# Kernel optimization log

Hardware: AMD Instinct MI355X
Metric: run time of the kernel (lower is better)

Reference implementation:

```python
import jax, jax.numpy as jnp
import numpy as np
from jax import lax

INPUT, HIDDEN, OUT = 64, 128, 40
B, T = 256, 512


def _lstm_layer(x, Wih, Whh, bih, bhh):
    # x: [B, T, D]; PyTorch gate order: i, f, g, o in stacked [4H, .] weights
    Bsz = x.shape[0]
    H = Whh.shape[1]
    b = bih + bhh

    def step(carry, xt):
        h, c = carry
        gates = xt @ Wih.T + h @ Whh.T + b  # [B, 4H]
        i, f, g, o = jnp.split(gates, 4, axis=-1)
        i = jax.nn.sigmoid(i)
        f = jax.nn.sigmoid(f)
        g = jnp.tanh(g)
        o = jax.nn.sigmoid(o)
        c = f * c + i * g
        h = o * jnp.tanh(c)
        return (h, c), h

    init = (jnp.zeros((Bsz, H), x.dtype), jnp.zeros((Bsz, H), x.dtype))
    (h_last, _), ys = lax.scan(step, init, jnp.swapaxes(x, 0, 1))
    return jnp.swapaxes(ys, 0, 1), h_last


def setup_inputs() -> dict:
    key = jax.random.key(0)
    ks = jax.random.split(key, 11)
    s_in = 1.0 / np.sqrt(HIDDEN)
    u = lambda k, shp: jax.random.uniform(k, shp, jnp.float32, -s_in, s_in)
    return {
        "x": jax.random.normal(ks[0], (B, T, INPUT), jnp.float32),
        "Wih0": u(ks[1], (4 * HIDDEN, INPUT)),
        "Whh0": u(ks[2], (4 * HIDDEN, HIDDEN)),
        "bih0": u(ks[3], (4 * HIDDEN,)),
        "bhh0": u(ks[4], (4 * HIDDEN,)),
        "Wih1": u(ks[5], (4 * HIDDEN, HIDDEN)),
        "Whh1": u(ks[6], (4 * HIDDEN, HIDDEN)),
        "bih1": u(ks[7], (4 * HIDDEN,)),
        "bhh1": u(ks[8], (4 * HIDDEN,)),
        "Wfc": u(ks[9], (OUT, HIDDEN)),
        "bfc": u(ks[10], (OUT,)),
    }


def reference(x, Wih0, Whh0, bih0, bhh0, Wih1, Whh1, bih1, bhh1, Wfc, bfc):
    y0, _ = _lstm_layer(x, Wih0, Whh0, bih0, bhh0)        # [B, T, H]
    _, h_last = _lstm_layer(y0, Wih1, Whh1, bih1, bhh1)   # [B, H] == y[:, -1]
    return h_last @ Wfc.T + bfc                            # [B, 40]
```

## Files before the change

kernel.cpp:

```cpp
#include <hip/hip_runtime.h>

#define BATCH 256
#define TLEN  512
#define DIN   64
#define HID   128
#define NOUT  40
#define SC    16

typedef _Float16 f16x8 __attribute__((ext_vector_type(8)));
typedef float    f32x4 __attribute__((ext_vector_type(4)));

#define MFMA16(a, b, c) __builtin_amdgcn_mfma_f32_16x16x32_f16((a), (b), (c), 0, 0, 0)

#define BARRIER() do {                                      \
    asm volatile("s_waitcnt lgkmcnt(0)" ::: "memory");      \
    __builtin_amdgcn_s_barrier();                           \
} while (0)

static __device__ __forceinline__ f16x8 pack8(float4 a, float4 b) {
    f16x8 v;
    v[0] = (_Float16)a.x; v[1] = (_Float16)a.y; v[2] = (_Float16)a.z; v[3] = (_Float16)a.w;
    v[4] = (_Float16)b.x; v[5] = (_Float16)b.y; v[6] = (_Float16)b.z; v[7] = (_Float16)b.w;
    return v;
}
static __device__ __forceinline__ float sig_(float x) {
    return __builtin_amdgcn_rcpf(1.0f + __expf(-x));
}
static __device__ __forceinline__ float tanh_(float x) {
    return fmaf(-2.0f, __builtin_amdgcn_rcpf(__expf(2.0f * x) + 1.0f), 1.0f);
}
static __device__ __forceinline__ f32x4 splat4(float v) { return (f32x4){v, v, v, v}; }

#define LD8(base, g, K, kt) pack8(*(const float4*)((base) + (size_t)(g) * (K) + (kt) * 32 + kg * 8), \
                                  *(const float4*)((base) + (size_t)(g) * (K) + (kt) * 32 + kg * 8 + 4))

#define H_STEP_CORE(SL, P)                                                      \
    f32x4 xi = *(const f32x4*)&xacc[((SL) * HID + hid) * 4];                    \
    const _Float16* hb = &h_lds[P][0];                                          \
    f16x8 h0 = *(const f16x8*)(hb + kg * 8);                                    \
    f16x8 h1 = *(const f16x8*)(hb + 32 + kg * 8);                               \
    f16x8 h2 = *(const f16x8*)(hb + 64 + kg * 8);                               \
    f16x8 h3 = *(const f16x8*)(hb + 96 + kg * 8);                               \
    f32x4 a0 = MFMA16(h0, Wh00, xi);                                            \
    f32x4 a1 = MFMA16(h0, Wh10, splat4(xi[1]));                                 \
    f32x4 a2 = MFMA16(h0, Wh20, splat4(xi[2]));                                 \
    f32x4 a3 = MFMA16(h0, Wh30, splat4(xi[3]));                                 \
    a0 = MFMA16(h1, Wh01, a0); a1 = MFMA16(h1, Wh11, a1);                       \
    a2 = MFMA16(h1, Wh21, a2); a3 = MFMA16(h1, Wh31, a3);                       \
    a0 = MFMA16(h2, Wh02, a0); a1 = MFMA16(h2, Wh12, a1);                       \
    a2 = MFMA16(h2, Wh22, a2); a3 = MFMA16(h2, Wh32, a3);                       \
    a0 = MFMA16(h3, Wh03, a0); a1 = MFMA16(h3, Wh13, a1);                       \
    a2 = MFMA16(h3, Wh23, a2); a3 = MFMA16(h3, Wh33, a3);                       \
    float iv = sig_(a0[0]), fv = sig_(a1[0]);                                   \
    float gv = tanh_(a2[0]), ov = sig_(a3[0]);                                  \
    cc = fmaf(fv, cc, iv * gv);                                                 \
    hv = ov * tanh_(cc);

__global__ void __attribute__((amdgpu_flat_work_group_size(512, 512), amdgpu_waves_per_eu(2, 2)))
lstm_l0(const float* __restrict__ x,
        const float* __restrict__ Wih, const float* __restrict__ Whh,
        const float* __restrict__ bih, const float* __restrict__ bhh,
        float* __restrict__ hstate, float* __restrict__ cstate,
        _Float16* __restrict__ y0, int t0, int t1)
{
    const int b    = blockIdx.x;
    const int tid  = threadIdx.x;
    const int lane = tid & 63;
    const int wave = tid >> 6;
    const int col  = lane & 15, kg = lane >> 4;
    const int hid  = wave * 16 + col;

    __shared__ __align__(16) float    xacc[SC * HID * 4];
    __shared__ __align__(16) _Float16 h_lds[2][HID];

    f16x8 Wx00 = LD8(Wih, 0 * HID + hid, DIN, 0), Wx01 = LD8(Wih, 0 * HID + hid, DIN, 1);
    f16x8 Wx10 = LD8(Wih, 1 * HID + hid, DIN, 0), Wx11 = LD8(Wih, 1 * HID + hid, DIN, 1);
    f16x8 Wx20 = LD8(Wih, 2 * HID + hid, DIN, 0), Wx21 = LD8(Wih, 2 * HID + hid, DIN, 1);
    f16x8 Wx30 = LD8(Wih, 3 * HID + hid, DIN, 0), Wx31 = LD8(Wih, 3 * HID + hid, DIN, 1);
    f16x8 Wh00 = LD8(Whh, 0 * HID + hid, HID, 0), Wh01 = LD8(Whh, 0 * HID + hid, HID, 1);
    f16x8 Wh02 = LD8(Whh, 0 * HID + hid, HID, 2), Wh03 = LD8(Whh, 0 * HID + hid, HID, 3);
    f16x8 Wh10 = LD8(Whh, 1 * HID + hid, HID, 0), Wh11 = LD8(Whh, 1 * HID + hid, HID, 1);
    f16x8 Wh12 = LD8(Whh, 1 * HID + hid, HID, 2), Wh13 = LD8(Whh, 1 * HID + hid, HID, 3);
    f16x8 Wh20 = LD8(Whh, 2 * HID + hid, HID, 0), Wh21 = LD8(Whh, 2 * HID + hid, HID, 1);
    f16x8 Wh22 = LD8(Whh, 2 * HID + hid, HID, 2), Wh23 = LD8(Whh, 2 * HID + hid, HID, 3);
    f16x8 Wh30 = LD8(Whh, 3 * HID + hid, HID, 0), Wh31 = LD8(Whh, 3 * HID + hid, HID, 1);
    f16x8 Wh32 = LD8(Whh, 3 * HID + hid, HID, 2), Wh33 = LD8(Whh, 3 * HID + hid, HID, 3);
    asm("" : "+a"(Wx00), "+a"(Wx01), "+a"(Wx10), "+a"(Wx11),
             "+a"(Wx20), "+a"(Wx21), "+a"(Wx30), "+a"(Wx31));
    asm("" : "+a"(Wh00), "+a"(Wh01), "+a"(Wh02), "+a"(Wh03),
             "+a"(Wh10), "+a"(Wh11), "+a"(Wh12), "+a"(Wh13));
    asm("" : "+a"(Wh20), "+a"(Wh21), "+a"(Wh22), "+a"(Wh23),
             "+a"(Wh30), "+a"(Wh31), "+a"(Wh32), "+a"(Wh33));

    const float bs0 = bih[0 * HID + hid] + bhh[0 * HID + hid];
    const float bs1 = bih[1 * HID + hid] + bhh[1 * HID + hid];
    const float bs2 = bih[2 * HID + hid] + bhh[2 * HID + hid];
    const float bs3 = bih[3 * HID + hid] + bhh[3 * HID + hid];

    float cc = cstate[(size_t)b * HID + hid];
    float hv = hstate[(size_t)b * HID + hid];
    if (kg == 0) h_lds[0][hid] = (_Float16)hv;

    const float* xA = x + (size_t)b * TLEN * DIN + (size_t)col * DIN + kg * 8;
    _Float16* y0p = y0 + (size_t)b * HID + hid;

    const int nt = t1 - t0;
    for (int sc = 0; sc < nt; sc += SC) {
        {
            const float* pa = xA + (size_t)(t0 + sc) * DIN;
            f16x8 A0 = pack8(*(const float4*)pa,        *(const float4*)(pa + 4));
            f16x8 A1 = pack8(*(const float4*)(pa + 32), *(const float4*)(pa + 36));
            f32x4 g0 = splat4(bs0), g1 = splat4(bs1), g2 = splat4(bs2), g3 = splat4(bs3);
            g0 = MFMA16(A0, Wx00, g0); g1 = MFMA16(A0, Wx10, g1);
            g2 = MFMA16(A0, Wx20, g2); g3 = MFMA16(A0, Wx30, g3);
            g0 = MFMA16(A1, Wx01, g0); g1 = MFMA16(A1, Wx11, g1);
            g2 = MFMA16(A1, Wx21, g2); g3 = MFMA16(A1, Wx31, g3);
            #pragma unroll
            for (int r = 0; r < 4; ++r) {
                const int tl = kg * 4 + r;
                float* d = &xacc[(tl * HID + hid) * 4];
                d[0] = g0[r]; d[1] = g1[r]; d[2] = g2[r]; d[3] = g3[r];
            }
        }
        BARRIER();
        for (int s = 0; s < SC; s += 2) {
            {
                H_STEP_CORE(s, 0)
                if (kg == 0) {
                    h_lds[1][hid] = (_Float16)hv;
                    y0p[(size_t)(sc + s) * (BATCH * HID)] = (_Float16)hv;
                }
                BARRIER();
            }
            {
                H_STEP_CORE(s + 1, 1)
                if (kg == 0) {
                    h_lds[0][hid] = (_Float16)hv;
                    y0p[(size_t)(sc + s + 1) * (BATCH * HID)] = (_Float16)hv;
                }
                BARRIER();
            }
        }
    }
    if (kg == 0) {
        cstate[(size_t)b * HID + hid] = cc;
        hstate[(size_t)b * HID + hid] = hv;
    }
}

__global__ void __attribute__((amdgpu_flat_work_group_size(512, 512), amdgpu_waves_per_eu(2, 2)))
lstm_l1(const _Float16* __restrict__ y0in,
        const float* __restrict__ Wih, const float* __restrict__ Whh,
        const float* __restrict__ bih, const float* __restrict__ bhh,
        float* __restrict__ hstate, float* __restrict__ cstate,
        int t0, int t1)
{
    const int b    = blockIdx.x;
    const int tid  = threadIdx.x;
    const int lane = tid & 63;
    const int wave = tid >> 6;
    const int col  = lane & 15, kg = lane >> 4;
    const int hid  = wave * 16 + col;

    __shared__ __align__(16) float    xacc[SC * HID * 4];
    __shared__ __align__(16) _Float16 h_lds[2][HID];

    f16x8 Wh00 = LD8(Whh, 0 * HID + hid, HID, 0), Wh01 = LD8(Whh, 0 * HID + hid, HID, 1);
    f16x8 Wh02 = LD8(Whh, 0 * HID + hid, HID, 2), Wh03 = LD8(Whh, 0 * HID + hid, HID, 3);
    f16x8 Wh10 = LD8(Whh, 1 * HID + hid, HID, 0), Wh11 = LD8(Whh, 1 * HID + hid, HID, 1);
    f16x8 Wh12 = LD8(Whh, 1 * HID + hid, HID, 2), Wh13 = LD8(Whh, 1 * HID + hid, HID, 3);
    f16x8 Wh20 = LD8(Whh, 2 * HID + hid, HID, 0), Wh21 = LD8(Whh, 2 * HID + hid, HID, 1);
    f16x8 Wh22 = LD8(Whh, 2 * HID + hid, HID, 2), Wh23 = LD8(Whh, 2 * HID + hid, HID, 3);
    f16x8 Wh30 = LD8(Whh, 3 * HID + hid, HID, 0), Wh31 = LD8(Whh, 3 * HID + hid, HID, 1);
    f16x8 Wh32 = LD8(Whh, 3 * HID + hid, HID, 2), Wh33 = LD8(Whh, 3 * HID + hid, HID, 3);
    asm("" : "+a"(Wh00), "+a"(Wh01), "+a"(Wh02), "+a"(Wh03),
             "+a"(Wh10), "+a"(Wh11), "+a"(Wh12), "+a"(Wh13));
    asm("" : "+a"(Wh20), "+a"(Wh21), "+a"(Wh22), "+a"(Wh23),
             "+a"(Wh30), "+a"(Wh31), "+a"(Wh32), "+a"(Wh33));

    const float bs0 = bih[0 * HID + hid] + bhh[0 * HID + hid];
    const float bs1 = bih[1 * HID + hid] + bhh[1 * HID + hid];
    const float bs2 = bih[2 * HID + hid] + bhh[2 * HID + hid];
    const float bs3 = bih[3 * HID + hid] + bhh[3 * HID + hid];

    float cc = cstate[(size_t)b * HID + hid];
    float hv = hstate[(size_t)b * HID + hid];
    if (kg == 0) h_lds[0][hid] = (_Float16)hv;

    const _Float16* yA = y0in + ((size_t)col * BATCH + b) * HID + kg * 8;

    const int nt = t1 - t0;
    for (int sc = 0; sc < nt; sc += SC) {
        {
            f16x8 Wy00 = LD8(Wih, 0 * HID + hid, HID, 0), Wy01 = LD8(Wih, 0 * HID + hid, HID, 1);
            f16x8 Wy02 = LD8(Wih, 0 * HID + hid, HID, 2), Wy03 = LD8(Wih, 0 * HID + hid, HID, 3);
            f16x8 Wy10 = LD8(Wih, 1 * HID + hid, HID, 0), Wy11 = LD8(Wih, 1 * HID + hid, HID, 1);
            f16x8 Wy12 = LD8(Wih, 1 * HID + hid, HID, 2), Wy13 = LD8(Wih, 1 * HID + hid, HID, 3);
            f16x8 Wy20 = LD8(Wih, 2 * HID + hid, HID, 0), Wy21 = LD8(Wih, 2 * HID + hid, HID, 1);
            f16x8 Wy22 = LD8(Wih, 2 * HID + hid, HID, 2), Wy23 = LD8(Wih, 2 * HID + hid, HID, 3);
            f16x8 Wy30 = LD8(Wih, 3 * HID + hid, HID, 0), Wy31 = LD8(Wih, 3 * HID + hid, HID, 1);
            f16x8 Wy32 = LD8(Wih, 3 * HID + hid, HID, 2), Wy33 = LD8(Wih, 3 * HID + hid, HID, 3);
            const _Float16* pa = yA + (size_t)sc * (BATCH * HID);
            f16x8 A0 = *(const f16x8*)(pa);
            f16x8 A1 = *(const f16x8*)(pa + 32);
            f16x8 A2 = *(const f16x8*)(pa + 64);
            f16x8 A3 = *(const f16x8*)(pa + 96);
            f32x4 g0 = splat4(bs0), g1 = splat4(bs1), g2 = splat4(bs2), g3 = splat4(bs3);
            g0 = MFMA16(A0, Wy00, g0); g1 = MFMA16(A0, Wy10, g1);
            g2 = MFMA16(A0, Wy20, g2); g3 = MFMA16(A0, Wy30, g3);
            g0 = MFMA16(A1, Wy01, g0); g1 = MFMA16(A1, Wy11, g1);
            g2 = MFMA16(A1, Wy21, g2); g3 = MFMA16(A1, Wy31, g3);
            g0 = MFMA16(A2, Wy02, g0); g1 = MFMA16(A2, Wy12, g1);
            g2 = MFMA16(A2, Wy22, g2); g3 = MFMA16(A2, Wy32, g3);
            g0 = MFMA16(A3, Wy03, g0); g1 = MFMA16(A3, Wy13, g1);
            g2 = MFMA16(A3, Wy23, g2); g3 = MFMA16(A3, Wy33, g3);
            #pragma unroll
            for (int r = 0; r < 4; ++r) {
                const int tl = kg * 4 + r;
                float* d = &xacc[(tl * HID + hid) * 4];
                d[0] = g0[r]; d[1] = g1[r]; d[2] = g2[r]; d[3] = g3[r];
            }
        }
        BARRIER();
        for (int s = 0; s < SC; s += 2) {
            {
                H_STEP_CORE(s, 0)
                if (kg == 0) h_lds[1][hid] = (_Float16)hv;
                BARRIER();
            }
            {
                H_STEP_CORE(s + 1, 1)
                if (kg == 0) h_lds[0][hid] = (_Float16)hv;
                BARRIER();
            }
        }
    }
    if (kg == 0) {
        cstate[(size_t)b * HID + hid] = cc;
        hstate[(size_t)b * HID + hid] = hv;
    }
}

__global__ __launch_bounds__(128) void fc_kernel(
    const float* __restrict__ h1, const float* __restrict__ Wfc,
    const float* __restrict__ bfc, float* __restrict__ out)
{
    const int b = blockIdx.x;
    const int o = threadIdx.x;
    __shared__ float hs[HID];
    hs[o] = h1[(size_t)b * HID + o];
    __syncthreads();
    if (o < NOUT) {
        const float4* w  = reinterpret_cast<const float4*>(Wfc + (size_t)o * HID);
        const float4* hv = reinterpret_cast<const float4*>(hs);
        float acc = bfc[o];
        #pragma unroll
        for (int q = 0; q < HID / 4; ++q) {
            float4 wv = w[q]; float4 h4 = hv[q];
            acc = fmaf(wv.x, h4.x, fmaf(wv.y, h4.y, fmaf(wv.z, h4.z, fmaf(wv.w, h4.w, acc))));
        }
        out[(size_t)b * NOUT + o] = acc;
    }
}

extern "C" void kernel_launch(void* const* d_in, const int* in_sizes, int n_in,
                              void* d_out, int out_size, void* d_ws, size_t ws_size,
                              hipStream_t stream) {
    const float* x    = (const float*)d_in[0];
    const float* Wih0 = (const float*)d_in[1];
    const float* Whh0 = (const float*)d_in[2];
    const float* bih0 = (const float*)d_in[3];
    const float* bhh0 = (const float*)d_in[4];
    const float* Wih1 = (const float*)d_in[5];
    const float* Whh1 = (const float*)d_in[6];
    const float* bih1 = (const float*)d_in[7];
    const float* bhh1 = (const float*)d_in[8];
    const float* Wfc  = (const float*)d_in[9];
    const float* bfc  = (const float*)d_in[10];
    float* out = (float*)d_out;

    float* hst0 = (float*)d_ws;
    float* cst0 = hst0 + BATCH * HID;
    float* hst1 = cst0 + BATCH * HID;
    float* cst1 = hst1 + BATCH * HID;
    _Float16* y0 = (_Float16*)(cst1 + BATCH * HID);

    const size_t stateBytes = (size_t)4 * BATCH * HID * sizeof(float);
    size_t avail = ws_size > stateBytes ? ws_size - stateBytes : 0;
    int Tc = (int)(avail / ((size_t)BATCH * HID * 2));
    if (Tc > TLEN) Tc = TLEN;
    Tc &= ~(SC - 1);
    if (Tc < SC) Tc = SC;

    hipMemsetAsync(d_ws, 0, stateBytes, stream);

    for (int t0 = 0; t0 < TLEN; t0 += Tc) {
        int t1 = t0 + Tc; if (t1 > TLEN) t1 = TLEN;
        lstm_l0<<<BATCH, 512, 0, stream>>>(x, Wih0, Whh0, bih0, bhh0, hst0, cst0, y0, t0, t1);
        lstm_l1<<<BATCH, 512, 0, stream>>>(y0, Wih1, Whh1, bih1, bhh1, hst1, cst1, t0, t1);
    }
    fc_kernel<<<BATCH, 128, 0, stream>>>(hst1, Wfc, bfc, out);
}
```

Baseline: 578.3 us.

## Give each wave two hidden-unit tiles and halve the LSTM block size

Both LSTM kernels now launch 256 threads (4 waves) instead of 512. Each wave computes two 16-wide hidden tiles, and all weights for both tiles stay in AGPRs. The recurrent MFMAs now start from zero accumulators, with the input projection added at the gate activations, and the next step's input-projection values are prefetched from LDS during the current step. This is meant to cut barrier and synchronisation cost per timestep and to give each wave eight independent MFMA chains instead of four. The cost is twice as many MFMAs per wave on the serial critical path and higher register pressure.

```diff
diff --git a/kernel.cpp b/kernel.cpp
--- a/kernel.cpp
+++ b/kernel.cpp
@@ -34,29 +34,37 @@
 #define LD8(base, g, K, kt) pack8(*(const float4*)((base) + (size_t)(g) * (K) + (kt) * 32 + kg * 8), \
                                   *(const float4*)((base) + (size_t)(g) * (K) + (kt) * 32 + kg * 8 + 4))
 
-#define H_STEP_CORE(SL, P)                                                      \
-    f32x4 xi = *(const f32x4*)&xacc[((SL) * HID + hid) * 4];                    \
+#define HROUND(H, KT)                                                           \
+    aA0 = MFMA16(H, WhA0_##KT, aA0); aA1 = MFMA16(H, WhA1_##KT, aA1);           \
+    aA2 = MFMA16(H, WhA2_##KT, aA2); aA3 = MFMA16(H, WhA3_##KT, aA3);           \
+    aB0 = MFMA16(H, WhB0_##KT, aB0); aB1 = MFMA16(H, WhB1_##KT, aB1);           \
+    aB2 = MFMA16(H, WhB2_##KT, aB2); aB3 = MFMA16(H, WhB3_##KT, aB3);
+
+#define H_STEP_CORE(S, P, XIA, XIB, XIAN, XIBN)                                 \
     const _Float16* hb = &h_lds[P][0];                                          \
     f16x8 h0 = *(const f16x8*)(hb + kg * 8);                                    \
     f16x8 h1 = *(const f16x8*)(hb + 32 + kg * 8);                               \
     f16x8 h2 = *(const f16x8*)(hb + 64 + kg * 8);                               \
     f16x8 h3 = *(const f16x8*)(hb + 96 + kg * 8);                               \
-    f32x4 a0 = MFMA16(h0, Wh00, xi);                                            \
-    f32x4 a1 = MFMA16(h0, Wh10, splat4(xi[1]));                                 \
-    f32x4 a2 = MFMA16(h0, Wh20, splat4(xi[2]));                                 \
-    f32x4 a3 = MFMA16(h0, Wh30, splat4(xi[3]));                                 \
-    a0 = MFMA16(h1, Wh01, a0); a1 = MFMA16(h1, Wh11, a1);                       \
-    a2 = MFMA16(h1, Wh21, a2); a3 = MFMA16(h1, Wh31, a3);                       \
-    a0 = MFMA16(h2, Wh02, a0); a1 = MFMA16(h2, Wh12, a1);                       \
-    a2 = MFMA16(h2, Wh22, a2); a3 = MFMA16(h2, Wh32, a3);                       \
-    a0 = MFMA16(h3, Wh03, a0); a1 = MFMA16(h3, Wh13, a1);                       \
-    a2 = MFMA16(h3, Wh23, a2); a3 = MFMA16(h3, Wh33, a3);                       \
-    float iv = sig_(a0[0]), fv = sig_(a1[0]);                                   \
-    float gv = tanh_(a2[0]), ov = sig_(a3[0]);                                  \
-    cc = fmaf(fv, cc, iv * gv);                                                 \
-    hv = ov * tanh_(cc);
-
-__global__ void __attribute__((amdgpu_flat_work_group_size(512, 512), amdgpu_waves_per_eu(2, 2)))
+    { int sn = (S) + 1 < SC ? (S) + 1 : SC - 1;                                 \
+      XIAN = *(const f32x4*)&xacc[(sn * HID + hidA) * 4];                       \
+      XIBN = *(const f32x4*)&xacc[(sn * HID + hidB) * 4]; }                     \
+    f32x4 aA0 = z4, aA1 = z4, aA2 = z4, aA3 = z4;                               \
+    f32x4 aB0 = z4, aB1 = z4, aB2 = z4, aB3 = z4;                               \
+    HROUND(h0, 0)                                                               \
+    HROUND(h1, 1)                                                               \
+    HROUND(h2, 2)                                                               \
+    HROUND(h3, 3)                                                               \
+    float ivA = sig_(aA0[0] + XIA[0]), fvA = sig_(aA1[0] + XIA[1]);             \
+    float gvA = tanh_(aA2[0] + XIA[2]), ovA = sig_(aA3[0] + XIA[3]);            \
+    ccA = fmaf(fvA, ccA, ivA * gvA);                                            \
+    hvA = ovA * tanh_(ccA);                                                     \
+    float ivB = sig_(aB0[0] + XIB[0]), fvB = sig_(aB1[0] + XIB[1]);             \
+    float gvB = tanh_(aB2[0] + XIB[2]), ovB = sig_(aB3[0] + XIB[3]);            \
+    ccB = fmaf(fvB, ccB, ivB * gvB);                                            \
+    hvB = ovB * tanh_(ccB);
+
+__global__ void __attribute__((amdgpu_flat_work_group_size(256, 256), amdgpu_waves_per_eu(1, 1)))
 lstm_l0(const float* __restrict__ x,
         const float* __restrict__ Wih, const float* __restrict__ Whh,
         const float* __restrict__ bih, const float* __restrict__ bhh,
@@ -68,41 +76,70 @@
     const int lane = tid & 63;
     const int wave = tid >> 6;
     const int col  = lane & 15, kg = lane >> 4;
-    const int hid  = wave * 16 + col;
+    const int hidA = wave * 32 + col;
+    const int hidB = hidA + 16;
 
     __shared__ __align__(16) float    xacc[SC * HID * 4];
     __shared__ __align__(16) _Float16 h_lds[2][HID];
 
-    f16x8 Wx00 = LD8(Wih, 0 * HID + hid, DIN, 0), Wx01 = LD8(Wih, 0 * HID + hid, DIN, 1);
-    f16x8 Wx10 = LD8(Wih, 1 * HID + hid, DIN, 0), Wx11 = LD8(Wih, 1 * HID + hid, DIN, 1);
-    f16x8 Wx20 = LD8(Wih, 2 * HID + hid, DIN, 0), Wx21 = LD8(Wih, 2 * HID + hid, DIN, 1);
-    f16x8 Wx30 = LD8(Wih, 3 * HID + hid, DIN, 0), Wx31 = LD8(Wih, 3 * HID + hid, DIN, 1);
-    f16x8 Wh00 = LD8(Whh, 0 * HID + hid, HID, 0), Wh01 = LD8(Whh, 0 * HID + hid, HID, 1);
-    f16x8 Wh02 = LD8(Whh, 0 * HID + hid, HID, 2), Wh03 = LD8(Whh, 0 * HID + hid, HID, 3);
-    f16x8 Wh10 = LD8(Whh, 1 * HID + hid, HID, 0), Wh11 = LD8(Whh, 1 * HID + hid, HID, 1);
-    f16x8 Wh12 = LD8(Whh, 1 * HID + hid, HID, 2), Wh13 = LD8(Whh, 1 * HID + hid, HID, 3);
-    f16x8 Wh20 = LD8(Whh, 2 * HID + hid, HID, 0), Wh21 = LD8(Whh, 2 * HID + hid, HID, 1);
-    f16x8 Wh22 = LD8(Whh, 2 * HID + hid, HID, 2), Wh23 = LD8(Whh, 2 * HID + hid, HID, 3);
-    f16x8 Wh30 = LD8(Whh, 3 * HID + hid, HID, 0), Wh31 = LD8(Whh, 3 * HID + hid, HID, 1);
-    f16x8 Wh32 = LD8(Whh, 3 * HID + hid, HID, 2), Wh33 = LD8(Whh, 3 * HID + hid, HID, 3);
-    asm("" : "+a"(Wx00), "+a"(Wx01), "+a"(Wx10), "+a"(Wx11),
-             "+a"(Wx20), "+a"(Wx21), "+a"(Wx30), "+a"(Wx31));
-    asm("" : "+a"(Wh00), "+a"(Wh01), "+a"(Wh02), "+a"(Wh03),
-             "+a"(Wh10), "+a"(Wh11), "+a"(Wh12), "+a"(Wh13));
-    asm("" : "+a"(Wh20), "+a"(Wh21), "+a"(Wh22), "+a"(Wh23),
-             "+a"(Wh30), "+a"(Wh31), "+a"(Wh32), "+a"(Wh33));
-
-    const float bs0 = bih[0 * HID + hid] + bhh[0 * HID + hid];
-    const float bs1 = bih[1 * HID + hid] + bhh[1 * HID + hid];
-    const float bs2 = bih[2 * HID + hid] + bhh[2 * HID + hid];
-    const float bs3 = bih[3 * HID + hid] + bhh[3 * HID + hid];
-
-    float cc = cstate[(size_t)b * HID + hid];
-    float hv = hstate[(size_t)b * HID + hid];
-    if (kg == 0) h_lds[0][hid] = (_Float16)hv;
+    f16x8 WxA0_0 = LD8(Wih, 0 * HID + hidA, DIN, 0), WxA0_1 = LD8(Wih, 0 * HID + hidA, DIN, 1);
+    f16x8 WxA1_0 = LD8(Wih, 1 * HID + hidA, DIN, 0), WxA1_1 = LD8(Wih, 1 * HID + hidA, DIN, 1);
+    f16x8 WxA2_0 = LD8(Wih, 2 * HID + hidA, DIN, 0), WxA2_1 = LD8(Wih, 2 * HID + hidA, DIN, 1);
+    f16x8 WxA3_0 = LD8(Wih, 3 * HID + hidA, DIN, 0), WxA3_1 = LD8(Wih, 3 * HID + hidA, DIN, 1);
+    f16x8 WxB0_0 = LD8(Wih, 0 * HID + hidB, DIN, 0), WxB0_1 = LD8(Wih, 0 * HID + hidB, DIN, 1);
+    f16x8 WxB1_0 = LD8(Wih, 1 * HID + hidB, DIN, 0), WxB1_1 = LD8(Wih, 1 * HID + hidB, DIN, 1);
+    f16x8 WxB2_0 = LD8(Wih, 2 * HID + hidB, DIN, 0), WxB2_1 = LD8(Wih, 2 * HID + hidB, DIN, 1);
+    f16x8 WxB3_0 = LD8(Wih, 3 * HID + hidB, DIN, 0), WxB3_1 = LD8(Wih, 3 * HID + hidB, DIN, 1);
+    f16x8 WhA0_0 = LD8(Whh, 0 * HID + hidA, HID, 0), WhA0_1 = LD8(Whh, 0 * HID + hidA, HID, 1);
+    f16x8 WhA0_2 = LD8(Whh, 0 * HID + hidA, HID, 2), WhA0_3 = LD8(Whh, 0 * HID + hidA, HID, 3);
+    f16x8 WhA1_0 = LD8(Whh, 1 * HID + hidA, HID, 0), WhA1_1 = LD8(Whh, 1 * HID + hidA, HID, 1);
+    f16x8 WhA1_2 = LD8(Whh, 1 * HID + hidA, HID, 2), WhA1_3 = LD8(Whh, 1 * HID + hidA, HID, 3);
+    f16x8 WhA2_0 = LD8(Whh, 2 * HID + hidA, HID, 0), WhA2_1 = LD8(Whh, 2 * HID + hidA, HID, 1);
+    f16x8 WhA2_2 = LD8(Whh, 2 * HID + hidA, HID, 2), WhA2_3 = LD8(Whh, 2 * HID + hidA, HID, 3);
+    f16x8 WhA3_0 = LD8(Whh, 3 * HID + hidA, HID, 0), WhA3_1 = LD8(Whh, 3 * HID + hidA, HID, 1);
+    f16x8 WhA3_2 = LD8(Whh, 3 * HID + hidA, HID, 2), WhA3_3 = LD8(Whh, 3 * HID + hidA, HID, 3);
+    f16x8 WhB0_0 = LD8(Whh, 0 * HID + hidB, HID, 0), WhB0_1 = LD8(Whh, 0 * HID + hidB, HID, 1);
+    f16x8 WhB0_2 = LD8(Whh, 0 * HID + hidB, HID, 2), WhB0_3 = LD8(Whh, 0 * HID + hidB, HID, 3);
+    f16x8 WhB1_0 = LD8(Whh, 1 * HID + hidB, HID, 0), WhB1_1 = LD8(Whh, 1 * HID + hidB, HID, 1);
+    f16x8 WhB1_2 = LD8(Whh, 1 * HID + hidB, HID, 2), WhB1_3 = LD8(Whh, 1 * HID + hidB, HID, 3);
+    f16x8 WhB2_0 = LD8(Whh, 2 * HID + hidB, HID, 0), WhB2_1 = LD8(Whh, 2 * HID + hidB, HID, 1);
+    f16x8 WhB2_2 = LD8(Whh, 2 * HID + hidB, HID, 2), WhB2_3 = LD8(Whh, 2 * HID + hidB, HID, 3);
+    f16x8 WhB3_0 = LD8(Whh, 3 * HID + hidB, HID, 0), WhB3_1 = LD8(Whh, 3 * HID + hidB, HID, 1);
+    f16x8 WhB3_2 = LD8(Whh, 3 * HID + hidB, HID, 2), WhB3_3 = LD8(Whh, 3 * HID + hidB, HID, 3);
+    asm("" : "+a"(WxA0_0), "+a"(WxA0_1), "+a"(WxA1_0), "+a"(WxA1_1),
+             "+a"(WxA2_0), "+a"(WxA2_1), "+a"(WxA3_0), "+a"(WxA3_1));
+    asm("" : "+a"(WxB0_0), "+a"(WxB0_1), "+a"(WxB1_0), "+a"(WxB1_1),
+             "+a"(WxB2_0), "+a"(WxB2_1), "+a"(WxB3_0), "+a"(WxB3_1));
+    asm("" : "+a"(WhA0_0), "+a"(WhA0_1), "+a"(WhA0_2), "+a"(WhA0_3),
+             "+a"(WhA1_0), "+a"(WhA1_1), "+a"(WhA1_2), "+a"(WhA1_3));
+    asm("" : "+a"(WhA2_0), "+a"(WhA2_1), "+a"(WhA2_2), "+a"(WhA2_3),
+             "+a"(WhA3_0), "+a"(WhA3_1), "+a"(WhA3_2), "+a"(WhA3_3));
+    asm("" : "+a"(WhB0_0), "+a"(WhB0_1), "+a"(WhB0_2), "+a"(WhB0_3),
+             "+a"(WhB1_0), "+a"(WhB1_1), "+a"(WhB1_2), "+a"(WhB1_3));
+    asm("" : "+a"(WhB2_0), "+a"(WhB2_1), "+a"(WhB2_2), "+a"(WhB2_3),
+             "+a"(WhB3_0), "+a"(WhB3_1), "+a"(WhB3_2), "+a"(WhB3_3));
+
+    const float bsA0 = bih[0 * HID + hidA] + bhh[0 * HID + hidA];
+    const float bsA1 = bih[1 * HID + hidA] + bhh[1 * HID + hidA];
+    const float bsA2 = bih[2 * HID + hidA] + bhh[2 * HID + hidA];
+    const float bsA3 = bih[3 * HID + hidA] + bhh[3 * HID + hidA];
+    const float bsB0 = bih[0 * HID + hidB] + bhh[0 * HID + hidB];
+    const float bsB1 = bih[1 * HID + hidB] + bhh[1 * HID + hidB];
+    const float bsB2 = bih[2 * HID + hidB] + bhh[2 * HID + hidB];
+    const float bsB3 = bih[3 * HID + hidB] + bhh[3 * HID + hidB];
+    const f32x4 z4 = {0.f, 0.f, 0.f, 0.f};
+
+    float ccA = cstate[(size_t)b * HID + hidA];
+    float ccB = cstate[(size_t)b * HID + hidB];
+    float hvA = hstate[(size_t)b * HID + hidA];
+    float hvB = hstate[(size_t)b * HID + hidB];
+    if (kg == 0) { h_lds[0][hidA] = (_Float16)hvA; h_lds[0][hidB] = (_Float16)hvB; }
 
     const float* xA = x + (size_t)b * TLEN * DIN + (size_t)col * DIN + kg * 8;
-    _Float16* y0p = y0 + (size_t)b * HID + hid;
+    _Float16* y0pA = y0 + (size_t)b * HID + hidA;
+    _Float16* y0pB = y0 + (size_t)b * HID + hidB;
+
+    f32x4 xiA0, xiB0, xiA1, xiB1;
 
     const int nt = t1 - t0;
     for (int sc = 0; sc < nt; sc += SC) {
@@ -110,45 +147,58 @@
             const float* pa = xA + (size_t)(t0 + sc) * DIN;
             f16x8 A0 = pack8(*(const float4*)pa,        *(const float4*)(pa + 4));
             f16x8 A1 = pack8(*(const float4*)(pa + 32), *(const float4*)(pa + 36));
-            f32x4 g0 = splat4(bs0), g1 = splat4(bs1), g2 = splat4(bs2), g3 = splat4(bs3);
-            g0 = MFMA16(A0, Wx00, g0); g1 = MFMA16(A0, Wx10, g1);
-            g2 = MFMA16(A0, Wx20, g2); g3 = MFMA16(A0, Wx30, g3);
-            g0 = MFMA16(A1, Wx01, g0); g1 = MFMA16(A1, Wx11, g1);
-            g2 = MFMA16(A1, Wx21, g2); g3 = MFMA16(A1, Wx31, g3);
+            f32x4 gA0 = splat4(bsA0), gA1 = splat4(bsA1), gA2 = splat4(bsA2), gA3 = splat4(bsA3);
+            f32x4 gB0 = splat4(bsB0), gB1 = splat4(bsB1), gB2 = splat4(bsB2), gB3 = splat4(bsB3);
+            gA0 = MFMA16(A0, WxA0_0, gA0); gA1 = MFMA16(A0, WxA1_0, gA1);
+            gA2 = MFMA16(A0, WxA2_0, gA2); gA3 = MFMA16(A0, WxA3_0, gA3);
+            gB0 = MFMA16(A0, WxB0_0, gB0); gB1 = MFMA16(A0, WxB1_0, gB1);
+            gB2 = MFMA16(A0, WxB2_0, gB2); gB3 = MFMA16(A0, WxB3_0, gB3);
+            gA0 = MFMA16(A1, WxA0_1, gA0); gA1 = MFMA16(A1, WxA1_1, gA1);
+            gA2 = MFMA16(A1, WxA2_1, gA2); gA3 = MFMA16(A1, WxA3_1, gA3);
+            gB0 = MFMA16(A1, WxB0_1, gB0); gB1 = MFMA16(A1, WxB1_1, gB1);
+            gB2 = MFMA16(A1, WxB2_1, gB2); gB3 = MFMA16(A1, WxB3_1, gB3);
             #pragma unroll
             for (int r = 0; r < 4; ++r) {
                 const int tl = kg * 4 + r;
-                float* d = &xacc[(tl * HID + hid) * 4];
-                d[0] = g0[r]; d[1] = g1[r]; d[2] = g2[r]; d[3] = g3[r];
+                *(float4*)&xacc[(tl * HID + hidA) * 4] = make_float4(gA0[r], gA1[r], gA2[r], gA3[r]);
+                *(float4*)&xacc[(tl * HID + hidB) * 4] = make_float4(gB0[r], gB1[r], gB2[r], gB3[r]);
             }
         }
         BARRIER();
+        xiA0 = *(const f32x4*)&xacc[(0 * HID + hidA) * 4];
+        xiB0 = *(const f32x4*)&xacc[(0 * HID + hidB) * 4];
         for (int s = 0; s < SC; s += 2) {
             {
-                H_STEP_CORE(s, 0)
+                H_STEP_CORE(s, 0, xiA0, xiB0, xiA1, xiB1)
                 if (kg == 0) {
-                    h_lds[1][hid] = (_Float16)hv;
-                    y0p[(size_t)(sc + s) * (BATCH * HID)] = (_Float16)hv;
+                    _Float16 hA = (_Float16)hvA, hB = (_Float16)hvB;
+                    h_lds[1][hidA] = hA; h_lds[1][hidB] = hB;
+                    y0pA[(size_t)(sc + s) * (BATCH * HID)] = hA;
+                    y0pB[(size_t)(sc + s) * (BATCH * HID)] = hB;
                 }
                 BARRIER();
             }
             {
-                H_STEP_CORE(s + 1, 1)
+                H_STEP_CORE(s + 1, 1, xiA1, xiB1, xiA0, xiB0)
                 if (kg == 0) {
-                    h_lds[0][hid] = (_Float16)hv;
-                    y0p[(size_t)(sc + s + 1) * (BATCH * HID)] = (_Float16)hv;
+                    _Float16 hA = (_Float16)hvA, hB = (_Float16)hvB;
+                    h_lds[0][hidA] = hA; h_lds[0][hidB] = hB;
+                    y0pA[(size_t)(sc + s + 1) * (BATCH * HID)] = hA;
+                    y0pB[(size_t)(sc + s + 1) * (BATCH * HID)] = hB;
                 }
                 BARRIER();
             }
         }
     }
     if (kg == 0) {
-        cstate[(size_t)b * HID + hid] = cc;
-        hstate[(size_t)b * HID + hid] = hv;
-    }
-}
-
-__global__ void __attribute__((amdgpu_flat_work_group_size(512, 512), amdgpu_waves_per_eu(2, 2)))
+        cstate[(size_t)b * HID + hidA] = ccA;
+        cstate[(size_t)b * HID + hidB] = ccB;
+        hstate[(size_t)b * HID + hidA] = hvA;
+        hstate[(size_t)b * HID + hidB] = hvB;
+    }
+}
+
+__global__ void __attribute__((amdgpu_flat_work_group_size(256, 256), amdgpu_waves_per_eu(1, 1)))
 lstm_l1(const _Float16* __restrict__ y0in,
         const float* __restrict__ Wih, const float* __restrict__ Whh,
         const float* __restrict__ bih, const float* __restrict__ bhh,
@@ -160,84 +210,133 @@
     const int lane = tid & 63;
     const int wave = tid >> 6;
     const int col  = lane & 15, kg = lane >> 4;
-    const int hid  = wave * 16 + col;
+    const int hidA = wave * 32 + col;
+    const int hidB = hidA + 16;
 
     __shared__ __align__(16) float    xacc[SC * HID * 4];
     __shared__ __align__(16) _Float16 h_lds[2][HID];
 
-    f16x8 Wh00 = LD8(Whh, 0 * HID + hid, HID, 0), Wh01 = LD8(Whh, 0 * HID + hid, HID, 1);
-    f16x8 Wh02 = LD8(Whh, 0 * HID + hid, HID, 2), Wh03 = LD8(Whh, 0 * HID + hid, HID, 3);
-    f16x8 Wh10 = LD8(Whh, 1 * HID + hid, HID, 0), Wh11 = LD8(Whh, 1 * HID + hid, HID, 1);
-    f16x8 Wh12 = LD8(Whh, 1 * HID + hid, HID, 2), Wh13 = LD8(Whh, 1 * HID + hid, HID, 3);
-    f16x8 Wh20 = LD8(Whh, 2 * HID + hid, HID, 0), Wh21 = LD8(Whh, 2 * HID + hid, HID, 1);
-    f16x8 Wh22 = LD8(Whh, 2 * HID + hid, HID, 2), Wh23 = LD8(Whh, 2 * HID + hid, HID, 3);
-    f16x8 Wh30 = LD8(Whh, 3 * HID + hid, HID, 0), Wh31 = LD8(Whh, 3 * HID + hid, HID, 1);
-    f16x8 Wh32 = LD8(Whh, 3 * HID + hid, HID, 2), Wh33 = LD8(Whh, 3 * HID + hid, HID, 3);
-    asm("" : "+a"(Wh00), "+a"(Wh01), "+a"(Wh02), "+a"(Wh03),
-             "+a"(Wh10), "+a"(Wh11), "+a"(Wh12), "+a"(Wh13));
-    asm("" : "+a"(Wh20), "+a"(Wh21), "+a"(Wh22), "+a"(Wh23),
-             "+a"(Wh30), "+a"(Wh31), "+a"(Wh32), "+a"(Wh33));
-
-    const float bs0 = bih[0 * HID + hid] + bhh[0 * HID + hid];
-    const float bs1 = bih[1 * HID + hid] + bhh[1 * HID + hid];
-    const float bs2 = bih[2 * HID + hid] + bhh[2 * HID + hid];
-    const float bs3 = bih[3 * HID + hid] + bhh[3 * HID + hid];
-
-    float cc = cstate[(size_t)b * HID + hid];
-    float hv = hstate[(size_t)b * HID + hid];
-    if (kg == 0) h_lds[0][hid] = (_Float16)hv;
+    f16x8 WhA0_0 = LD8(Whh, 0 * HID + hidA, HID, 0), WhA0_1 = LD8(Whh, 0 * HID + hidA, HID, 1);
+    f16x8 WhA0_2 = LD8(Whh, 0 * HID + hidA, HID, 2), WhA0_3 = LD8(Whh, 0 * HID + hidA, HID, 3);
+    f16x8 WhA1_0 = LD8(Whh, 1 * HID + hidA, HID, 0), WhA1_1 = LD8(Whh, 1 * HID + hidA, HID, 1);
+    f16x8 WhA1_2 = LD8(Whh, 1 * HID + hidA, HID, 2), WhA1_3 = LD8(Whh, 1 * HID + hidA, HID, 3);
+    f16x8 WhA2_0 = LD8(Whh, 2 * HID + hidA, HID, 0), WhA2_1 = LD8(Whh, 2 * HID + hidA, HID, 1);
+    f16x8 WhA2_2 = LD8(Whh, 2 * HID + hidA, HID, 2), WhA2_3 = LD8(Whh, 2 * HID + hidA, HID, 3);
+    f16x8 WhA3_0 = LD8(Whh, 3 * HID + hidA, HID, 0), WhA3_1 = LD8(Whh, 3 * HID + hidA, HID, 1);
+    f16x8 WhA3_2 = LD8(Whh, 3 * HID + hidA, HID, 2), WhA3_3 = LD8(Whh, 3 * HID + hidA, HID, 3);
+    f16x8 WhB0_0 = LD8(Whh, 0 * HID + hidB, HID, 0), WhB0_1 = LD8(Whh, 0 * HID + hidB, HID, 1);
+    f16x8 WhB0_2 = LD8(Whh, 0 * HID + hidB, HID, 2), WhB0_3 = LD8(Whh, 0 * HID + hidB, HID, 3);
+    f16x8 WhB1_0 = LD8(Whh, 1 * HID + hidB, HID, 0), WhB1_1 = LD8(Whh, 1 * HID + hidB, HID, 1);
+    f16x8 WhB1_2 = LD8(Whh, 1 * HID + hidB, HID, 2), WhB1_3 = LD8(Whh, 1 * HID + hidB, HID, 3);
+    f16x8 WhB2_0 = LD8(Whh, 2 * HID + hidB, HID, 0), WhB2_1 = LD8(Whh, 2 * HID + hidB, HID, 1);
+    f16x8 WhB2_2 = LD8(Whh, 2 * HID + hidB, HID, 2), WhB2_3 = LD8(Whh, 2 * HID + hidB, HID, 3);
+    f16x8 WhB3_0 = LD8(Whh, 3 * HID + hidB, HID, 0), WhB3_1 = LD8(Whh, 3 * HID + hidB, HID, 1);
+    f16x8 WhB3_2 = LD8(Whh, 3 * HID + hidB, HID, 2), WhB3_3 = LD8(Whh, 3 * HID + hidB, HID, 3);
+    asm("" : "+a"(WhA0_0), "+a"(WhA0_1), "+a"(WhA0_2), "+a"(WhA0_3),
+             "+a"(WhA1_0), "+a"(WhA1_1), "+a"(WhA1_2), "+a"(WhA1_3));
+    asm("" : "+a"(WhA2_0), "+a"(WhA2_1), "+a"(WhA2_2), "+a"(WhA2_3),
+             "+a"(WhA3_0), "+a"(WhA3_1), "+a"(WhA3_2), "+a"(WhA3_3));
+    asm("" : "+a"(WhB0_0), "+a"(WhB0_1), "+a"(WhB0_2), "+a"(WhB0_3),
+             "+a"(WhB1_0), "+a"(WhB1_1), "+a"(WhB1_2), "+a"(WhB1_3));
+    asm("" : "+a"(WhB2_0), "+a"(WhB2_1), "+a"(WhB2_2), "+a"(WhB2_3),
+             "+a"(WhB3_0), "+a"(WhB3_1), "+a"(WhB3_2), "+a"(WhB3_3));
+
+    const float bsA0 = bih[0 * HID + hidA] + bhh[0 * HID + hidA];
+    const float bsA1 = bih[1 * HID + hidA] + bhh[1 * HID + hidA];
+    const float bsA2 = bih[2 * HID + hidA] + bhh[2 * HID + hidA];
+    const float bsA3 = bih[3 * HID + hidA] + bhh[3 * HID + hidA];
+    const float bsB0 = bih[0 * HID + hidB] + bhh[0 * HID + hidB];
+    const float bsB1 = bih[1 * HID + hidB] + bhh[1 * HID + hidB];
+    const float bsB2 = bih[2 * HID + hidB] + bhh[2 * HID + hidB];
+    const float bsB3 = bih[3 * HID + hidB] + bhh[3 * HID + hidB];
+    const f32x4 z4 = {0.f, 0.f, 0.f, 0.f};
+
+    float ccA = cstate[(size_t)b * HID + hidA];
+    float ccB = cstate[(size_t)b * HID + hidB];
+    float hvA = hstate[(size_t)b * HID + hidA];
+    float hvB = hstate[(size_t)b * HID + hidB];
+    if (kg == 0) { h_lds[0][hidA] = (_Float16)hvA; h_lds[0][hidB] = (_Float16)hvB; }
 
     const _Float16* yA = y0in + ((size_t)col * BATCH + b) * HID + kg * 8;
+
+    f32x4 xiA0, xiB0, xiA1, xiB1;
 
     const int nt = t1 - t0;
     for (int sc = 0; sc < nt; sc += SC) {
         {
-            f16x8 Wy00 = LD8(Wih, 0 * HID + hid, HID, 0), Wy01 = LD8(Wih, 0 * HID + hid, HID, 1);
-            f16x8 Wy02 = LD8(Wih, 0 * HID + hid, HID, 2), Wy03 = LD8(Wih, 0 * HID + hid, HID, 3);
-            f16x8 Wy10 = LD8(Wih, 1 * HID + hid, HID, 0), Wy11 = LD8(Wih, 1 * HID + hid, HID, 1);
-            f16x8 Wy12 = LD8(Wih, 1 * HID + hid, HID, 2), Wy13 = LD8(Wih, 1 * HID + hid, HID, 3);
-            f16x8 Wy20 = LD8(Wih, 2 * HID + hid, HID, 0), Wy21 = LD8(Wih, 2 * HID + hid, HID, 1);
-            f16x8 Wy22 = LD8(Wih, 2 * HID + hid, HID, 2), Wy23 = LD8(Wih, 2 * HID + hid, HID, 3);
-            f16x8 Wy30 = LD8(Wih, 3 * HID + hid, HID, 0), Wy31 = LD8(Wih, 3 * HID + hid, HID, 1);
-            f16x8 Wy32 = LD8(Wih, 3 * HID + hid, HID, 2), Wy33 = LD8(Wih, 3 * HID + hid, HID, 3);
+            f16x8 WyA0_0 = LD8(Wih, 0 * HID + hidA, HID, 0), WyA0_1 = LD8(Wih, 0 * HID + hidA, HID, 1);
+            f16x8 WyA0_2 = LD8(Wih, 0 * HID + hidA, HID, 2), WyA0_3 = LD8(Wih, 0 * HID + hidA, HID, 3);
+            f16x8 WyA1_0 = LD8(Wih, 1 * HID + hidA, HID, 0), WyA1_1 = LD8(Wih, 1 * HID + hidA, HID, 1);
+            f16x8 WyA1_2 = LD8(Wih, 1 * HID + hidA, HID, 2), WyA1_3 = LD8(Wih, 1 * HID + hidA, HID, 3);
+            f16x8 WyA2_0 = LD8(Wih, 2 * HID + hidA, HID, 0), WyA2_1 = LD8(Wih, 2 * HID + hidA, HID, 1);
+            f16x8 WyA2_2 = LD8(Wih, 2 * HID + hidA, HID, 2), WyA2_3 = LD8(Wih, 2 * HID + hidA, HID, 3);
+            f16x8 WyA3_0 = LD8(Wih, 3 * HID + hidA, HID, 0), WyA3_1 = LD8(Wih, 3 * HID + hidA, HID, 1);
+            f16x8 WyA3_2 = LD8(Wih, 3 * HID + hidA, HID, 2), WyA3_3 = LD8(Wih, 3 * HID + hidA, HID, 3);
+            f16x8 WyB0_0 = LD8(Wih, 0 * HID + hidB, HID, 0), WyB0_1 = LD8(Wih, 0 * HID + hidB, HID, 1);
+            f16x8 WyB0_2 = LD8(Wih, 0 * HID + hidB, HID, 2), WyB0_3 = LD8(Wih, 0 * HID + hidB, HID, 3);
+            f16x8 WyB1_0 = LD8(Wih, 1 * HID + hidB, HID, 0), WyB1_1 = LD8(Wih, 1 * HID + hidB, HID, 1);
+            f16x8 WyB1_2 = LD8(Wih, 1 * HID + hidB, HID, 2), WyB1_3 = LD8(Wih, 1 * HID + hidB, HID, 3);
+            f16x8 WyB2_0 = LD8(Wih, 2 * HID + hidB, HID, 0), WyB2_1 = LD8(Wih, 2 * HID + hidB, HID, 1);
+            f16x8 WyB2_2 = LD8(Wih, 2 * HID + hidB, HID, 2), WyB2_3 = LD8(Wih, 2 * HID + hidB, HID, 3);
+            f16x8 WyB3_0 = LD8(Wih, 3 * HID + hidB, HID, 0), WyB3_1 = LD8(Wih, 3 * HID + hidB, HID, 1);
+            f16x8 WyB3_2 = LD8(Wih, 3 * HID + hidB, HID, 2), WyB3_3 = LD8(Wih, 3 * HID + hidB, HID, 3);
             const _Float16* pa = yA + (size_t)sc * (BATCH * HID);
             f16x8 A0 = *(const f16x8*)(pa);
             f16x8 A1 = *(const f16x8*)(pa + 32);
             f16x8 A2 = *(const f16x8*)(pa + 64);
             f16x8 A3 = *(const f16x8*)(pa + 96);
-            f32x4 g0 = splat4(bs0), g1 = splat4(bs1), g2 = splat4(bs2), g3 = splat4(bs3);
-            g0 = MFMA16(A0, Wy00, g0); g1 = MFMA16(A0, Wy10, g1);
-            g2 = MFMA16(A0, Wy20, g2); g3 = MFMA16(A0, Wy30, g3);
-            g0 = MFMA16(A1, Wy01, g0); g1 = MFMA16(A1, Wy11, g1);
-            g2 = MFMA16(A1, Wy21, g2); g3 = MFMA16(A1, Wy31, g3);
-            g0 = MFMA16(A2, Wy02, g0); g1 = MFMA16(A2, Wy12, g1);
-            g2 = MFMA16(A2, Wy22, g2); g3 = MFMA16(A2, Wy32, g3);
-            g0 = MFMA16(A3, Wy03, g0); g1 = MFMA16(A3, Wy13, g1);
-            g2 = MFMA16(A3, Wy23, g2); g3 = MFMA16(A3, Wy33, g3);
+            f32x4 gA0 = splat4(bsA0), gA1 = splat4(bsA1), gA2 = splat4(bsA2), gA3 = splat4(bsA3);
+            f32x4 gB0 = splat4(bsB0), gB1 = splat4(bsB1), gB2 = splat4(bsB2), gB3 = splat4(bsB3);
+            gA0 = MFMA16(A0, WyA0_0, gA0); gA1 = MFMA16(A0, WyA1_0, gA1);
+            gA2 = MFMA16(A0, WyA2_0, gA2); gA3 = MFMA16(A0, WyA3_0, gA3);
+            gB0 = MFMA16(A0, WyB0_0, gB0); gB1 = MFMA16(A0, WyB1_0, gB1);
+            gB2 = MFMA16(A0, WyB2_0, gB2); gB3 = MFMA16(A0, WyB3_0, gB3);
+            gA0 = MFMA16(A1, WyA0_1, gA0); gA1 = MFMA16(A1, WyA1_1, gA1);
+            gA2 = MFMA16(A1, WyA2_1, gA2); gA3 = MFMA16(A1, WyA3_1, gA3);
+            gB0 = MFMA16(A1, WyB0_1, gB0); gB1 = MFMA16(A1, WyB1_1, gB1);
+            gB2 = MFMA16(A1, WyB2_1, gB2); gB3 = MFMA16(A1, WyB3_1, gB3);
+            gA0 = MFMA16(A2, WyA0_2, gA0); gA1 = MFMA16(A2, WyA1_2, gA1);
+            gA2 = MFMA16(A2, WyA2_2, gA2); gA3 = MFMA16(A2, WyA3_2, gA3);
+            gB0 = MFMA16(A2, WyB0_2, gB0); gB1 = MFMA16(A2, WyB1_2, gB1);
+            gB2 = MFMA16(A2, WyB2_2, gB2); gB3 = MFMA16(A2, WyB3_2, gB3);
+            gA0 = MFMA16(A3, WyA0_3, gA0); gA1 = MFMA16(A3, WyA1_3, gA1);
+            gA2 = MFMA16(A3, WyA2_3, gA2); gA3 = MFMA16(A3, WyA3_3, gA3);
+            gB0 = MFMA16(A3, WyB0_3, gB0); gB1 = MFMA16(A3, WyB1_3, gB1);
+            gB2 = MFMA16(A3, WyB2_3, gB2); gB3 = MFMA16(A3, WyB3_3, gB3);
             #pragma unroll
             for (int r = 0; r < 4; ++r) {
                 const int tl = kg * 4 + r;
-                float* d = &xacc[(tl * HID + hid) * 4];
-                d[0] = g0[r]; d[1] = g1[r]; d[2] = g2[r]; d[3] = g3[r];
+                *(float4*)&xacc[(tl * HID + hidA) * 4] = make_float4(gA0[r], gA1[r], gA2[r], gA3[r]);
+                *(float4*)&xacc[(tl * HID + hidB) * 4] = make_float4(gB0[r], gB1[r], gB2[r], gB3[r]);
             }
         }
         BARRIER();
+        xiA0 = *(const f32x4*)&xacc[(0 * HID + hidA) * 4];
+        xiB0 = *(const f32x4*)&xacc[(0 * HID + hidB) * 4];
         for (int s = 0; s < SC; s += 2) {
             {
-                H_STEP_CORE(s, 0)
-                if (kg == 0) h_lds[1][hid] = (_Float16)hv;
+                H_STEP_CORE(s, 0, xiA0, xiB0, xiA1, xiB1)
+                if (kg == 0) {
+                    h_lds[1][hidA] = (_Float16)hvA;
+                    h_lds[1][hidB] = (_Float16)hvB;
+                }
                 BARRIER();
             }
             {
-                H_STEP_CORE(s + 1, 1)
-                if (kg == 0) h_lds[0][hid] = (_Float16)hv;
+                H_STEP_CORE(s + 1, 1, xiA1, xiB1, xiA0, xiB0)
+                if (kg == 0) {
+                    h_lds[0][hidA] = (_Float16)hvA;
+                    h_lds[0][hidB] = (_Float16)hvB;
+                }
                 BARRIER();
             }
         }
     }
     if (kg == 0) {
-        cstate[(size_t)b * HID + hid] = cc;
-        hstate[(size_t)b * HID + hid] = hv;
+        cstate[(size_t)b * HID + hidA] = ccA;
+        cstate[(size_t)b * HID + hidB] = ccB;
+        hstate[(size_t)b * HID + hidA] = hvA;
+        hstate[(size_t)b * HID + hidB] = hvB;
     }
 }
 
@@ -296,8 +395,8 @@
 
     for (int t0 = 0; t0 < TLEN; t0 += Tc) {
         int t1 = t0 + Tc; if (t1 > TLEN) t1 = TLEN;
-        lstm_l0<<<BATCH, 512, 0, stream>>>(x, Wih0, Whh0, bih0, bhh0, hst0, cst0, y0, t0, t1);
-        lstm_l1<<<BATCH, 512, 0, stream>>>(y0, Wih1, Whh1, bih1, bhh1, hst1, cst1, t0, t1);
+        lstm_l0<<<BATCH, 256, 0, stream>>>(x, Wih0, Whh0, bih0, bhh0, hst0, cst0, y0, t0, t1);
+        lstm_l1<<<BATCH, 256, 0, stream>>>(y0, Wih1, Whh1, bih1, bhh1, hst1, cst1, t0, t1);
     }
     fc_kernel<<<BATCH, 128, 0, stream>>>(hst1, Wfc, bfc, out);
 }
```

New measurement: 583.1 us. About the same (+0.8%).
